# Performance work log

Hardware: AMD Instinct MI355X
Metric: run time of the kernel (lower is better)

The kernel has to match this reference:

```python
import math
import jax, jax.numpy as jnp
import numpy as np

NO_ITEMS = 50000
EMB_DIM = 448
FEAT_DIM = 64
DIM = EMB_DIM + FEAT_DIM  # 512
N_BLOCKS = 2
B, S = 8, 2048
EPS = 1e-05


def setup_inputs() -> dict:
    key = jax.random.key(0)
    ks = jax.random.split(key, 16)
    inv = 1.0 / math.sqrt(DIM)
    inp = {
        "user_sequence": jax.random.randint(ks[0], (B, S), 0, NO_ITEMS),
        "user_sequence_features": jax.random.normal(ks[1], (B, S, FEAT_DIM), dtype=jnp.float32),
        "emb_table": jax.random.normal(ks[2], (NO_ITEMS, EMB_DIM), dtype=jnp.float32) * 0.02,
        # stacked per-block params [L, DIM, DIM] / [L, DIM]; torch Linear: y = x @ W.T + b
        "Wq": jax.random.normal(ks[3], (N_BLOCKS, DIM, DIM), dtype=jnp.float32) * inv,
        "bq": jax.random.normal(ks[4], (N_BLOCKS, DIM), dtype=jnp.float32) * inv,
        "Wk": jax.random.normal(ks[5], (N_BLOCKS, DIM, DIM), dtype=jnp.float32) * inv,
        "bk": jax.random.normal(ks[6], (N_BLOCKS, DIM), dtype=jnp.float32) * inv,
        "Wv": jax.random.normal(ks[7], (N_BLOCKS, DIM, DIM), dtype=jnp.float32) * inv,
        "bv": jax.random.normal(ks[8], (N_BLOCKS, DIM), dtype=jnp.float32) * inv,
        "W1": jax.random.normal(ks[9], (N_BLOCKS, DIM, DIM), dtype=jnp.float32) * inv,
        "b1": jax.random.normal(ks[10], (N_BLOCKS, DIM), dtype=jnp.float32) * inv,
        "W2": jax.random.normal(ks[11], (N_BLOCKS, DIM, DIM), dtype=jnp.float32) * inv,
        "b2": jax.random.normal(ks[12], (N_BLOCKS, DIM), dtype=jnp.float32) * inv,
    }
    return inp


def _seq_norm(h):
    # EmbeddingSequenceNorm: normalize over sequence axis (axis=1),
    # torch .std() is unbiased (ddof=1); note the double eps in the source.
    mean = h.mean(axis=1)                        # [B, D]
    std = jnp.std(h, axis=1, ddof=1) + 1e-05     # [B, D]
    return (h - mean[:, None, :]) / (std[:, None, :] + EPS)


def reference(user_sequence, user_sequence_features, emb_table,
              Wq, bq, Wk, bk, Wv, bv, W1, b1, W2, b2):
    emb = emb_table[user_sequence]                       # [B, S, EMB_DIM]
    feats = user_sequence_features[:, :, :FEAT_DIM]      # [B, S, FEAT_DIM]
    x = jnp.concatenate([emb, feats], axis=-1)           # [B, S, DIM]
    scale = 1.0 / math.sqrt(DIM)
    for l in range(N_BLOCKS):
        q = x @ Wq[l].T + bq[l]
        k = x @ Wk[l].T + bk[l]
        v = x @ Wv[l].T + bv[l]
        # NOTE: no softmax in the original — raw tril(QK^T * scale) @ V
        scores = jnp.einsum('bqd,bkd->bqk', q, k) * scale  # [B, S, S]
        scores = jnp.tril(scores)
        h = jnp.einsum('bqk,bkd->bqd', scores, v)
        h = _seq_norm(h)
        h = jnp.maximum(h @ W1[l].T + b1[l], 0.0) @ W2[l].T + b2[l]
        x = h
    return x[:, -1]  # [B, DIM]
```

## Files before the change

### kernel.cpp

```cpp
#include <hip/hip_runtime.h>
#include <hip/hip_bf16.h>

typedef __hip_bfloat16 BF;
typedef __bf16 v8bf __attribute__((ext_vector_type(8)));
typedef float v4f __attribute__((ext_vector_type(4)));

constexpr int SEQ = 2048;
constexpr int DIMC = 512;
constexpr int BSZ = 8;

#define GF_RELU 1
#define GF_CAUSAL 2
#define GF_KCAP 4
#define GF_QKV 8
#define GF_BATCH8 16

#define WAIT_VM4 0x0F74
#define WAIT_VM0 0x0F70

__device__ __forceinline__ void async16(BF* lds, const BF* g) {
  __builtin_amdgcn_global_load_lds(
      (const __attribute__((address_space(1))) void*)g,
      (__attribute__((address_space(3))) void*)lds,
      16, 0, 0);
}

__global__ __launch_bounds__(256, 4) void gemm_bt(
    const BF* __restrict__ A, const BF* __restrict__ W, const float* __restrict__ bias,
    BF* __restrict__ outB, float* __restrict__ outF, BF* __restrict__ outV,
    int M, int N, int K, int nbx,
    long long strideA, long long strideW, long long strideC,
    float scale, int flags)
{
  const int id = blockIdx.x;
  int z, bx, by;
  if (flags & GF_BATCH8) {
    z = id & 7;
    const int t = id >> 3;
    bx = t % nbx;
    by = t / nbx;
  } else {
    z = 0;
    by = (id & 7) + ((id >> 3) & 15) * 8;
    bx = id >> 7;
  }
  const int m0 = by * 128;
  const int n0 = bx * 128;
  if ((flags & GF_CAUSAL) && n0 > m0) return;

  const BF* __restrict__ Ab = A + (size_t)z * strideA;
  const BF* __restrict__ Wb = W + (size_t)z * strideW;
  const size_t coff = (size_t)z * strideC;

  const int tid = threadIdx.x;
  const int w = tid >> 6;
  const int lane = tid & 63;
  const int lane15 = lane & 15;
  const int quad = lane >> 4;
  const int wr = w >> 1, wc = w & 1;
  const int rl = lane >> 2;
  const int clsw = ((lane & 3) ^ ((rl >> 1) & 3)) << 3;

  __shared__ __align__(16) BF sA[2][128 * 32];
  __shared__ __align__(16) BF sW[2][128 * 32];

  v4f acc[4][4];
  {
    v4f zero = {0.f, 0.f, 0.f, 0.f};
#pragma unroll
    for (int a = 0; a < 4; ++a)
#pragma unroll
      for (int b = 0; b < 4; ++b) acc[a][b] = zero;
  }

  int Klim = K;
  if (flags & GF_KCAP) { int kc = m0 + 128; if (kc < Klim) Klim = kc; }
  const int ksteps = Klim >> 5;

  auto stage = [&](int kk, int buf) {
    const int k0 = kk << 5;
#pragma unroll
    for (int i = 0; i < 2; ++i) {
      const int r0 = w * 32 + i * 16;
      async16(&sA[buf][r0 * 32], Ab + (size_t)(m0 + r0 + rl) * K + (k0 + clsw));
      async16(&sW[buf][r0 * 32], Wb + (size_t)(n0 + r0 + rl) * K + (k0 + clsw));
    }
  };

  stage(0, 0);
  const int sw = quad ^ ((lane15 >> 1) & 3);

  for (int kk = 0; kk < ksteps; ++kk) {
    const int cur = kk & 1;
    if (kk + 1 < ksteps) {
      stage(kk + 1, cur ^ 1);
      __builtin_amdgcn_s_waitcnt(WAIT_VM4);
    } else {
      __builtin_amdgcn_s_waitcnt(WAIT_VM0);
    }
    __builtin_amdgcn_s_barrier();

    v8bf aF[4], wF[4];
    const v8bf* sAv = (const v8bf*)sA[cur];
    const v8bf* sWv = (const v8bf*)sW[cur];
#pragma unroll
    for (int t = 0; t < 4; ++t) {
      aF[t] = sAv[(wr * 64 + t * 16 + lane15) * 4 + sw];
      wF[t] = sWv[(wc * 64 + t * 16 + lane15) * 4 + sw];
    }
#pragma unroll
    for (int mt = 0; mt < 4; ++mt)
#pragma unroll
      for (int nt = 0; nt < 4; ++nt)
        acc[mt][nt] = __builtin_amdgcn_mfma_f32_16x16x32_bf16(aF[mt], wF[nt], acc[mt][nt], 0, 0, 0);
    __builtin_amdgcn_s_barrier();
  }

#pragma unroll
  for (int mt = 0; mt < 4; ++mt) {
    const int rb = m0 + wr * 64 + mt * 16 + quad * 4;
#pragma unroll
    for (int nt = 0; nt < 4; ++nt) {
      const int cg = n0 + wc * 64 + nt * 16 + lane15;
      const float bv = bias ? bias[cg] : 0.0f;
#pragma unroll
      for (int i = 0; i < 4; ++i) {
        const int rg = rb + i;
        float v = acc[mt][nt][i] * scale + bv;
        if ((flags & GF_RELU) && v < 0.f) v = 0.f;
        if ((flags & GF_CAUSAL) && cg > rg) v = 0.f;
        if (flags & GF_QKV) {
          const BF b = __float2bfloat16(v);
          if (cg < 512) outB[(size_t)rg * 512 + cg] = b;
          else if (cg < 1024) ((BF*)outF)[(size_t)rg * 512 + (cg - 512)] = b;
          else outV[(size_t)rg * 512 + (cg - 1024)] = b;
        } else {
          if (outB) outB[coff + (size_t)rg * N + cg] = __float2bfloat16(v);
          if (outF) outF[coff + (size_t)rg * N + cg] = v;
        }
      }
    }
  }
}

__global__ void gather_kernel(const int* __restrict__ seq, const float* __restrict__ feats,
                              const float* __restrict__ emb, BF* __restrict__ xb) {
  const int row = blockIdx.x;
  const int t = threadIdx.x;
  const int idx = seq[row];
  BF* xr = xb + (size_t)row * DIMC;
  if (t < 224) {
    const float2 e = *(const float2*)(emb + (size_t)idx * 448 + t * 2);
    xr[t * 2] = __float2bfloat16(e.x);
    xr[t * 2 + 1] = __float2bfloat16(e.y);
  } else {
    const int j = (t - 224) * 2;
    const float2 f = *(const float2*)(feats + (size_t)row * 64 + j);
    xr[448 + j] = __float2bfloat16(f.x);
    xr[448 + j + 1] = __float2bfloat16(f.y);
  }
}

__global__ void prep_kernel(const float* __restrict__ W1, const float* __restrict__ W2,
                            const float* __restrict__ Wq, const float* __restrict__ Wk,
                            const float* __restrict__ Wv, const float* __restrict__ bq,
                            const float* __restrict__ bk, const float* __restrict__ bv,
                            BF* __restrict__ wb, BF* __restrict__ wqkv, float* __restrict__ bqkv) {
  const int t = blockIdx.x * 256 + threadIdx.x;
  const long long i = (long long)t * 4;
  float4 v;
  BF* o;
  if (i < 1048576) {
    v = (i < 524288) ? *(const float4*)(W1 + i) : *(const float4*)(W2 + (i - 524288));
    o = wb + i;
  } else {
    const long long j = i - 1048576;
    const int l = j >= 786432 ? 1 : 0;
    const long long rem = j - (long long)l * 786432;
    const int r = (int)(rem >> 9), c = (int)(rem & 511);
    const float* s = (r < 512) ? Wq : (r < 1024 ? Wk : Wv);
    v = *(const float4*)(s + (size_t)l * 262144 + (size_t)(r & 511) * 512 + c);
    o = wqkv + j;
  }
  o[0] = __float2bfloat16(v.x); o[1] = __float2bfloat16(v.y);
  o[2] = __float2bfloat16(v.z); o[3] = __float2bfloat16(v.w);
  if (t < 768) {
#pragma unroll
    for (int e = t * 4; e < t * 4 + 4; ++e) {
      const int l = e / 1536, r = e % 1536;
      const float* s = (r < 512) ? bq : (r < 1024 ? bk : bv);
      bqkv[e] = s[l * 512 + (r & 511)];
    }
  }
}

__global__ void transpose_kernel(const BF* __restrict__ in, BF* __restrict__ out) {
  __shared__ BF t[64][65];
  const int b = blockIdx.z;
  const int s0 = blockIdx.x * 64, d0 = blockIdx.y * 64;
  const int dx = threadIdx.x & 63, ry = threadIdx.x >> 6;
  const BF* ib = in + ((size_t)b * SEQ + s0) * DIMC + d0;
  BF* ob = out + ((size_t)b * DIMC + d0) * SEQ + s0;
#pragma unroll
  for (int i = 0; i < 16; ++i)
    t[ry + i * 4][dx] = ib[(size_t)(ry + i * 4) * DIMC + dx];
  __syncthreads();
#pragma unroll
  for (int i = 0; i < 16; ++i)
    ob[(size_t)(ry + i * 4) * SEQ + dx] = t[dx][ry + i * 4];
}

__global__ void seqsum_kernel(const float* __restrict__ h, float* __restrict__ part) {
  const int b = blockIdx.y, ch = blockIdx.x;
  const int t = threadIdx.x;
  const int half = t >> 7, cidx = t & 127;
  const float* hb = h + ((size_t)b * SEQ + ch * 64 + half * 32) * DIMC + cidx * 4;
  float4 sum = {0.f, 0.f, 0.f, 0.f}, sq = {0.f, 0.f, 0.f, 0.f};
#pragma unroll 4
  for (int r = 0; r < 32; ++r) {
    const float4 v = *(const float4*)(hb + (size_t)r * DIMC);
    sum.x += v.x; sum.y += v.y; sum.z += v.z; sum.w += v.w;
    sq.x += v.x * v.x; sq.y += v.y * v.y; sq.z += v.z * v.z; sq.w += v.w * v.w;
  }
  __shared__ float4 lsum[256], lsq[256];
  lsum[t] = sum; lsq[t] = sq;
  __syncthreads();
  if (t < 128) {
    const float4 s2 = lsum[t + 128], q2 = lsq[t + 128];
    sum.x += s2.x; sum.y += s2.y; sum.z += s2.z; sum.w += s2.w;
    sq.x += q2.x; sq.y += q2.y; sq.z += q2.z; sq.w += q2.w;
    float* ps = part + (size_t)(b * 32 + ch) * 1024;
    *(float4*)(ps + cidx * 4) = sum;
    *(float4*)(ps + 512 + cidx * 4) = sq;
  }
}

__global__ void seqstat_kernel(const float* __restrict__ part, float2* __restrict__ stat) {
  const int i = blockIdx.x * 256 + threadIdx.x;
  const int b = i >> 9, d = i & 511;
  const float* p = part + (size_t)b * 32 * 1024 + d;
  float s = 0.f, q = 0.f;
#pragma unroll 8
  for (int c = 0; c < 32; ++c) { s += p[c * 1024]; q += p[c * 1024 + 512]; }
  const float mean = s / SEQ;
  float var = (q - mean * s) / (SEQ - 1);
  if (var < 0.f) var = 0.f;
  stat[i] = make_float2(mean, 1.0f / (sqrtf(var) + 2e-5f));
}

__global__ void seqapply_kernel(const float* __restrict__ h, const float2* __restrict__ stat,
                                BF* __restrict__ out) {
  const size_t i = ((size_t)blockIdx.x * 256 + threadIdx.x) * 4;
  const int b = (int)(i >> 20);
  const int d = (int)(i & 511);
  const float4 v = *(const float4*)(h + i);
  const float2* sb = stat + (b << 9) + d;
  const float4 s01 = *(const float4*)(sb);
  const float4 s23 = *(const float4*)(sb + 2);
  out[i]     = __float2bfloat16((v.x - s01.x) * s01.y);
  out[i + 1] = __float2bfloat16((v.y - s01.z) * s01.w);
  out[i + 2] = __float2bfloat16((v.z - s23.x) * s23.y);
  out[i + 3] = __float2bfloat16((v.w - s23.z) * s23.w);
}

__global__ void ffn1last_kernel(const float* __restrict__ h32, const float2* __restrict__ stat,
                                const BF* __restrict__ W1B, const float* __restrict__ b1,
                                float* __restrict__ f1g) {
  const int b = blockIdx.x >> 3, nb = blockIdx.x & 7;
  const int t = threadIdx.x;
  __shared__ float hn[512];
  const float* hr = h32 + ((size_t)b * SEQ + (SEQ - 1)) * DIMC;
  const float2* sb = stat + b * 512;
  for (int d = t; d < 512; d += 256) {
    const float2 s = sb[d];
    hn[d] = (hr[d] - s.x) * s.y;
  }
  __syncthreads();
  const int o = nb * 64 + (t >> 2);
  const int seg = t & 3;
  const BF* wr = W1B + (size_t)o * 512 + seg * 128;
  const float* hs = hn + seg * 128;
  float acc = 0.f;
#pragma unroll
  for (int j = 0; j < 128; j += 8) {
    const v8bf wv = *(const v8bf*)(wr + j);
#pragma unroll
    for (int e = 0; e < 8; ++e) acc += hs[j + e] * (float)wv[e];
  }
  acc += __shfl_xor(acc, 1, 64);
  acc += __shfl_xor(acc, 2, 64);
  if (seg == 0) {
    const float v = acc + b1[o];
    f1g[b * 512 + o] = v > 0.f ? v : 0.f;
  }
}

__global__ void ffn2last_kernel(const float* __restrict__ f1g, const BF* __restrict__ W2B,
                                const float* __restrict__ b2, float* __restrict__ out) {
  const int b = blockIdx.x >> 3, nb = blockIdx.x & 7;
  const int t = threadIdx.x;
  __shared__ float f1[512];
  const float* fr = f1g + b * 512;
  for (int d = t; d < 512; d += 256) f1[d] = fr[d];
  __syncthreads();
  const int o = nb * 64 + (t >> 2);
  const int seg = t & 3;
  const BF* wr = W2B + (size_t)o * 512 + seg * 128;
  const float* fs = f1 + seg * 128;
  float acc = 0.f;
#pragma unroll
  for (int j = 0; j < 128; j += 8) {
    const v8bf wv = *(const v8bf*)(wr + j);
#pragma unroll
    for (int e = 0; e < 8; ++e) acc += fs[j + e] * (float)wv[e];
  }
  acc += __shfl_xor(acc, 1, 64);
  acc += __shfl_xor(acc, 2, 64);
  if (seg == 0) out[b * 512 + o] = acc + b2[o];
}

extern "C" void kernel_launch(void* const* d_in, const int* in_sizes, int n_in,
                              void* d_out, int out_size, void* d_ws, size_t ws_size,
                              hipStream_t stream) {
  const int* seq = (const int*)d_in[0];
  const float* feats = (const float*)d_in[1];
  const float* emb = (const float*)d_in[2];
  const float* Wq = (const float*)d_in[3];
  const float* bq = (const float*)d_in[4];
  const float* Wk = (const float*)d_in[5];
  const float* bk = (const float*)d_in[6];
  const float* Wv = (const float*)d_in[7];
  const float* bv = (const float*)d_in[8];
  const float* W1 = (const float*)d_in[9];
  const float* b1 = (const float*)d_in[10];
  const float* W2 = (const float*)d_in[11];
  const float* b2 = (const float*)d_in[12];
  float* out = (float*)d_out;

  char* ws = (char*)d_ws;
  const size_t MB = 1024 * 1024;
  BF* xb = (BF*)(ws);
  BF* qb = (BF*)(ws + 16 * MB);
  BF* kb = (BF*)(ws + 32 * MB);
  BF* vt = (BF*)(ws + 48 * MB);
  float* h32 = (float*)(ws + 64 * MB);
  BF* vtmp = (BF*)(ws + 64 * MB);
  BF* sc = (BF*)(ws + 96 * MB);
  BF* wb = (BF*)(ws + 160 * MB);
  BF* wqkv = (BF*)(ws + 162 * MB);
  float* bqkv = (float*)(ws + 166 * MB);
  float* f1g = (float*)(ws + 166 * MB + 512 * 1024);
  float* part = (float*)(ws + 167 * MB);
  float2* stat = (float2*)(ws + 168 * MB);

  const int WT = 2 * 512 * 512;
  prep_kernel<<<2560, 256, 0, stream>>>(W1, W2, Wq, Wk, Wv, bq, bk, bv, wb, wqkv, bqkv);
  gather_kernel<<<BSZ * SEQ, 256, 0, stream>>>(seq, feats, emb, xb);

  const float attn_scale = 0.04419417382415922f;
  const dim3 blk(256);

  for (int l = 0; l < 2; ++l) {
    const BF* W1B = wb + (size_t)l * 262144;
    const BF* W2B = wb + (size_t)WT + (size_t)l * 262144;

    gemm_bt<<<1536, blk, 0, stream>>>(xb, wqkv + (size_t)l * 786432, bqkv + l * 1536,
        qb, (float*)kb, vtmp, 16384, 1536, 512, 12, 0, 0, 0, 1.0f, GF_QKV);
    transpose_kernel<<<dim3(32, 8, 8), blk, 0, stream>>>(vtmp, vt);
    gemm_bt<<<2048, blk, 0, stream>>>(qb, kb, nullptr, sc, nullptr, nullptr,
        2048, 2048, 512, 16,
        (long long)SEQ * DIMC, (long long)SEQ * DIMC, (long long)SEQ * SEQ,
        attn_scale, GF_CAUSAL | GF_BATCH8);
    gemm_bt<<<512, blk, 0, stream>>>(sc, vt, nullptr, nullptr, h32, nullptr,
        2048, 512, 2048, 4,
        (long long)SEQ * SEQ, (long long)DIMC * SEQ, (long long)SEQ * DIMC,
        1.0f, GF_KCAP | GF_BATCH8);
    seqsum_kernel<<<dim3(32, 8), blk, 0, stream>>>(h32, part);
    seqstat_kernel<<<16, 256, 0, stream>>>(part, stat);

    if (l == 0) {
      seqapply_kernel<<<16384, 256, 0, stream>>>(h32, stat, qb);
      gemm_bt<<<512, blk, 0, stream>>>(qb, W1B, b1 + l * 512, kb, nullptr, nullptr,
          16384, 512, 512, 4, 0, 0, 0, 1.0f, GF_RELU);
      gemm_bt<<<512, blk, 0, stream>>>(kb, W2B, b2 + l * 512, xb,
          nullptr, nullptr, 16384, 512, 512, 4, 0, 0, 0, 1.0f, 0);
    } else {
      ffn1last_kernel<<<64, blk, 0, stream>>>(h32, stat, W1B, b1 + 512, f1g);
      ffn2last_kernel<<<64, blk, 0, stream>>>(f1g, W2B, b2 + 512, out);
    }
  }
}
```

Baseline: 523.0 us.

## Add 256x128-tile GEMM variant with 512 threads for QKV and QK^T

Adds gemm_bt2, a 512-thread, 8-wave GEMM that computes a 256x128 output tile per block instead of 128x128, and uses it for the fused QKV projection and the causal QK^T score GEMM. Each W tile loaded into LDS is now shared across twice as many A rows, which cuts global and LDS traffic per output and halves the block count. The larger blocks use more LDS and registers, which can reduce occupancy. The causal skip now works at 256-row granularity, so some tiles above the diagonal that were skipped before are now computed.

```diff
diff --git a/kernel.cpp b/kernel.cpp
--- a/kernel.cpp
+++ b/kernel.cpp
@@ -16,6 +16,7 @@
 #define GF_BATCH8 16
 
 #define WAIT_VM4 0x0F74
+#define WAIT_VM3 0x0F73
 #define WAIT_VM0 0x0F70
 
 __device__ __forceinline__ void async16(BF* lds, const BF* g) {
@@ -95,6 +96,125 @@
     if (kk + 1 < ksteps) {
       stage(kk + 1, cur ^ 1);
       __builtin_amdgcn_s_waitcnt(WAIT_VM4);
+    } else {
+      __builtin_amdgcn_s_waitcnt(WAIT_VM0);
+    }
+    __builtin_amdgcn_s_barrier();
+
+    v8bf aF[4], wF[4];
+    const v8bf* sAv = (const v8bf*)sA[cur];
+    const v8bf* sWv = (const v8bf*)sW[cur];
+#pragma unroll
+    for (int t = 0; t < 4; ++t) {
+      aF[t] = sAv[(wr * 64 + t * 16 + lane15) * 4 + sw];
+      wF[t] = sWv[(wc * 64 + t * 16 + lane15) * 4 + sw];
+    }
+#pragma unroll
+    for (int mt = 0; mt < 4; ++mt)
+#pragma unroll
+      for (int nt = 0; nt < 4; ++nt)
+        acc[mt][nt] = __builtin_amdgcn_mfma_f32_16x16x32_bf16(aF[mt], wF[nt], acc[mt][nt], 0, 0, 0);
+    __builtin_amdgcn_s_barrier();
+  }
+
+#pragma unroll
+  for (int mt = 0; mt < 4; ++mt) {
+    const int rb = m0 + wr * 64 + mt * 16 + quad * 4;
+#pragma unroll
+    for (int nt = 0; nt < 4; ++nt) {
+      const int cg = n0 + wc * 64 + nt * 16 + lane15;
+      const float bv = bias ? bias[cg] : 0.0f;
+#pragma unroll
+      for (int i = 0; i < 4; ++i) {
+        const int rg = rb + i;
+        float v = acc[mt][nt][i] * scale + bv;
+        if ((flags & GF_RELU) && v < 0.f) v = 0.f;
+        if ((flags & GF_CAUSAL) && cg > rg) v = 0.f;
+        if (flags & GF_QKV) {
+          const BF b = __float2bfloat16(v);
+          if (cg < 512) outB[(size_t)rg * 512 + cg] = b;
+          else if (cg < 1024) ((BF*)outF)[(size_t)rg * 512 + (cg - 512)] = b;
+          else outV[(size_t)rg * 512 + (cg - 1024)] = b;
+        } else {
+          if (outB) outB[coff + (size_t)rg * N + cg] = __float2bfloat16(v);
+          if (outF) outF[coff + (size_t)rg * N + cg] = v;
+        }
+      }
+    }
+  }
+}
+
+__global__ __launch_bounds__(512, 6) void gemm_bt2(
+    const BF* __restrict__ A, const BF* __restrict__ W, const float* __restrict__ bias,
+    BF* __restrict__ outB, float* __restrict__ outF, BF* __restrict__ outV,
+    int N, int K,
+    long long strideA, long long strideW, long long strideC,
+    float scale, int flags)
+{
+  const int id = blockIdx.x;
+  int z, bx, by;
+  if (flags & GF_BATCH8) {
+    z = id & 7;
+    const int t = id >> 3;
+    bx = t & 15;
+    by = t >> 4;
+  } else {
+    z = 0;
+    by = (id & 7) + 8 * ((id >> 3) & 7);
+    bx = id >> 6;
+  }
+  const int m0 = by << 8;
+  const int n0 = bx << 7;
+  if ((flags & GF_CAUSAL) && n0 > m0 + 255) return;
+
+  const BF* __restrict__ Ab = A + (size_t)z * strideA;
+  const BF* __restrict__ Wb = W + (size_t)z * strideW;
+  const size_t coff = (size_t)z * strideC;
+
+  const int tid = threadIdx.x;
+  const int w = tid >> 6;
+  const int lane = tid & 63;
+  const int lane15 = lane & 15;
+  const int quad = lane >> 4;
+  const int wr = w >> 1, wc = w & 1;
+  const int rl = lane >> 2;
+  const int clsw = ((lane & 3) ^ ((rl >> 1) & 3)) << 3;
+
+  __shared__ __align__(16) BF sA[2][256 * 32];
+  __shared__ __align__(16) BF sW[2][128 * 32];
+
+  v4f acc[4][4];
+  {
+    v4f zero = {0.f, 0.f, 0.f, 0.f};
+#pragma unroll
+    for (int a = 0; a < 4; ++a)
+#pragma unroll
+      for (int b = 0; b < 4; ++b) acc[a][b] = zero;
+  }
+
+  int Klim = K;
+  if (flags & GF_KCAP) { int kc = m0 + 256; if (kc < Klim) Klim = kc; }
+  const int ksteps = Klim >> 5;
+
+  auto stage = [&](int kk, int buf) {
+    const int k0 = kk << 5;
+#pragma unroll
+    for (int i = 0; i < 2; ++i) {
+      const int r0 = w * 32 + i * 16;
+      async16(&sA[buf][r0 * 32], Ab + (size_t)(m0 + r0 + rl) * K + (k0 + clsw));
+    }
+    const int r1 = w * 16;
+    async16(&sW[buf][r1 * 32], Wb + (size_t)(n0 + r1 + rl) * K + (k0 + clsw));
+  };
+
+  stage(0, 0);
+  const int sw = quad ^ ((lane15 >> 1) & 3);
+
+  for (int kk = 0; kk < ksteps; ++kk) {
+    const int cur = kk & 1;
+    if (kk + 1 < ksteps) {
+      stage(kk + 1, cur ^ 1);
+      __builtin_amdgcn_s_waitcnt(WAIT_VM3);
     } else {
       __builtin_amdgcn_s_waitcnt(WAIT_VM0);
     }
@@ -364,11 +484,11 @@
     const BF* W1B = wb + (size_t)l * 262144;
     const BF* W2B = wb + (size_t)WT + (size_t)l * 262144;
 
-    gemm_bt<<<1536, blk, 0, stream>>>(xb, wqkv + (size_t)l * 786432, bqkv + l * 1536,
-        qb, (float*)kb, vtmp, 16384, 1536, 512, 12, 0, 0, 0, 1.0f, GF_QKV);
+    gemm_bt2<<<768, 512, 0, stream>>>(xb, wqkv + (size_t)l * 786432, bqkv + l * 1536,
+        qb, (float*)kb, vtmp, 1536, 512, 0, 0, 0, 1.0f, GF_QKV);
     transpose_kernel<<<dim3(32, 8, 8), blk, 0, stream>>>(vtmp, vt);
-    gemm_bt<<<2048, blk, 0, stream>>>(qb, kb, nullptr, sc, nullptr, nullptr,
-        2048, 2048, 512, 16,
+    gemm_bt2<<<1024, 512, 0, stream>>>(qb, kb, nullptr, sc, nullptr, nullptr,
+        2048, 512,
         (long long)SEQ * DIMC, (long long)SEQ * DIMC, (long long)SEQ * SEQ,
         attn_scale, GF_CAUSAL | GF_BATCH8);
     gemm_bt<<<512, blk, 0, stream>>>(sc, vt, nullptr, nullptr, h32, nullptr,
```

Result: slower. 957.3 us (+83.0%).

## Stage bf16 GEMM epilogue through LDS for vectorized stores; reverse KCAP block order

Applied to the files above, without the earlier changes.

The bf16-output GEMM epilogue now writes the accumulator tile into shared memory with an XOR swizzle, then stores to global memory as coalesced 16-byte vectors. Before, each thread wrote scattered 2-byte elements. This reuses the staging buffers, which are merged into one array, and adds one extra barrier per block. Separately, batched K-capped launches now map blocks in reverse row order so the longest causal blocks are scheduled first, which should reduce tail imbalance.

```diff
diff --git a/kernel.cpp b/kernel.cpp
--- a/kernel.cpp
+++ b/kernel.cpp
@@ -39,6 +39,7 @@
     const int t = id >> 3;
     bx = t % nbx;
     by = t / nbx;
+    if (flags & GF_KCAP) by = (M >> 7) - 1 - by;
   } else {
     z = 0;
     by = (id & 7) + ((id >> 3) & 15) * 8;
@@ -61,8 +62,9 @@
   const int rl = lane >> 2;
   const int clsw = ((lane & 3) ^ ((rl >> 1) & 3)) << 3;
 
-  __shared__ __align__(16) BF sA[2][128 * 32];
-  __shared__ __align__(16) BF sW[2][128 * 32];
+  __shared__ __align__(16) BF smem[16384];
+  BF* sA = smem;
+  BF* sW = smem + 8192;
 
   v4f acc[4][4];
   {
@@ -82,8 +84,8 @@
 #pragma unroll
     for (int i = 0; i < 2; ++i) {
       const int r0 = w * 32 + i * 16;
-      async16(&sA[buf][r0 * 32], Ab + (size_t)(m0 + r0 + rl) * K + (k0 + clsw));
-      async16(&sW[buf][r0 * 32], Wb + (size_t)(n0 + r0 + rl) * K + (k0 + clsw));
+      async16(&sA[buf * 4096 + r0 * 32], Ab + (size_t)(m0 + r0 + rl) * K + (k0 + clsw));
+      async16(&sW[buf * 4096 + r0 * 32], Wb + (size_t)(n0 + r0 + rl) * K + (k0 + clsw));
     }
   };
 
@@ -101,8 +103,8 @@
     __builtin_amdgcn_s_barrier();
 
     v8bf aF[4], wF[4];
-    const v8bf* sAv = (const v8bf*)sA[cur];
-    const v8bf* sWv = (const v8bf*)sW[cur];
+    const v8bf* sAv = (const v8bf*)(sA + cur * 4096);
+    const v8bf* sWv = (const v8bf*)(sW + cur * 4096);
 #pragma unroll
     for (int t = 0; t < 4; ++t) {
       aF[t] = sAv[(wr * 64 + t * 16 + lane15) * 4 + sw];
@@ -116,25 +118,59 @@
     __builtin_amdgcn_s_barrier();
   }
 
-#pragma unroll
-  for (int mt = 0; mt < 4; ++mt) {
-    const int rb = m0 + wr * 64 + mt * 16 + quad * 4;
-#pragma unroll
-    for (int nt = 0; nt < 4; ++nt) {
-      const int cg = n0 + wc * 64 + nt * 16 + lane15;
-      const float bv = bias ? bias[cg] : 0.0f;
-#pragma unroll
-      for (int i = 0; i < 4; ++i) {
-        const int rg = rb + i;
-        float v = acc[mt][nt][i] * scale + bv;
-        if ((flags & GF_RELU) && v < 0.f) v = 0.f;
-        if ((flags & GF_CAUSAL) && cg > rg) v = 0.f;
-        if (flags & GF_QKV) {
-          const BF b = __float2bfloat16(v);
-          if (cg < 512) outB[(size_t)rg * 512 + cg] = b;
-          else if (cg < 1024) ((BF*)outF)[(size_t)rg * 512 + (cg - 512)] = b;
-          else outV[(size_t)rg * 512 + (cg - 1024)] = b;
-        } else {
+  if ((flags & GF_QKV) || (outB && !outF)) {
+#pragma unroll
+    for (int mt = 0; mt < 4; ++mt) {
+#pragma unroll
+      for (int nt = 0; nt < 4; ++nt) {
+        const int col = wc * 64 + nt * 16 + lane15;
+        const int cg = n0 + col;
+        const float bv = bias ? bias[cg] : 0.0f;
+#pragma unroll
+        for (int i = 0; i < 4; ++i) {
+          const int row = wr * 64 + mt * 16 + quad * 4 + i;
+          float v = acc[mt][nt][i] * scale + bv;
+          if ((flags & GF_RELU) && v < 0.f) v = 0.f;
+          if ((flags & GF_CAUSAL) && cg > m0 + row) v = 0.f;
+          smem[row * 128 + ((((col >> 3) ^ ((row >> 2) & 3)) << 3) | (col & 7))] =
+              __float2bfloat16(v);
+        }
+      }
+    }
+    __syncthreads();
+    BF* dst;
+    int ldc, coloff;
+    if (flags & GF_QKV) {
+      const int seg = n0 >> 9;
+      dst = (seg == 0) ? outB : (seg == 1 ? (BF*)outF : outV);
+      ldc = 512;
+      coloff = n0 & 511;
+    } else {
+      dst = outB + coff;
+      ldc = N;
+      coloff = n0;
+    }
+#pragma unroll
+    for (int p = 0; p < 8; ++p) {
+      const int g = p * 256 + tid;
+      const int row = g >> 4, ch = g & 15;
+      const v8bf val = *(const v8bf*)(smem + row * 128 + ((ch ^ ((row >> 2) & 3)) << 3));
+      *(v8bf*)(dst + (size_t)(m0 + row) * ldc + coloff + ch * 8) = val;
+    }
+  } else {
+#pragma unroll
+    for (int mt = 0; mt < 4; ++mt) {
+      const int rb = m0 + wr * 64 + mt * 16 + quad * 4;
+#pragma unroll
+      for (int nt = 0; nt < 4; ++nt) {
+        const int cg = n0 + wc * 64 + nt * 16 + lane15;
+        const float bv = bias ? bias[cg] : 0.0f;
+#pragma unroll
+        for (int i = 0; i < 4; ++i) {
+          const int rg = rb + i;
+          float v = acc[mt][nt][i] * scale + bv;
+          if ((flags & GF_RELU) && v < 0.f) v = 0.f;
+          if ((flags & GF_CAUSAL) && cg > rg) v = 0.f;
           if (outB) outB[coff + (size_t)rg * N + cg] = __float2bfloat16(v);
           if (outF) outF[coff + (size_t)rg * N + cg] = v;
         }
```

New measurement: 445.8 us. 14.8% less time.
